# Kernel optimization log

Measured on AMD Instinct MI355X. Metric: run time of the kernel, lower is better.

Reference implementation:

```python
import jax, jax.numpy as jnp
import numpy as np

N_VERT = 1000          # num_of_vertices; x has 3*N_VERT rows
B = 32                 # batch
IN_DIM = 64
OUT_DIMS = [64, 64, 64]


def setup_inputs() -> dict:
    key = jax.random.key(0)
    ks = jax.random.split(key, 8)
    threeN = 3 * N_VERT
    x = jax.random.normal(ks[0], (threeN, B, IN_DIM), dtype=jnp.float32)
    # dense (normalized-ish) adjacency over the localized spatio-temporal graph
    adj = jax.random.uniform(ks[1], (threeN, threeN), dtype=jnp.float32) / threeN
    inp = {"x": x, "adj": adj}
    in_d = IN_DIM
    for i, out_d in enumerate(OUT_DIMS):
        # torch Linear(in_d, 2*out_d): store as [in_d, 2*out_d] for x @ W + b
        scale = 1.0 / np.sqrt(in_d)
        inp[f"W{i}"] = jax.random.uniform(ks[2 + 2 * i], (in_d, 2 * out_d),
                                          minval=-scale, maxval=scale, dtype=jnp.float32)
        inp[f"b{i}"] = jax.random.uniform(ks[3 + 2 * i], (2 * out_d,),
                                          minval=-scale, maxval=scale, dtype=jnp.float32)
        in_d = out_d
    return inp


def _gcn_glu(adj, x, W, b, out_dim):
    # aggregate: [3N,3N] x [3N,B,C] -> [3N,B,C]
    h = jnp.einsum('nm,mbc->nbc', adj, x)
    lr = h @ W + b                       # [3N,B,2*out]
    lhs, rhs = lr[..., :out_dim], lr[..., out_dim:]
    return lhs * jax.nn.sigmoid(rhs)     # GLU


def reference(x, adj, W0, b0, W1, b1, W2, b2):
    n = x.shape[0] // 3
    Ws = [(W0, b0), (W1, b1), (W2, b2)]
    mids = []
    h = x
    for (W, b), out_d in zip(Ws, OUT_DIMS):
        h = _gcn_glu(adj, h, W, b, out_d)
        mids.append(h[n:2 * n])          # middle time-step slice [N,B,out]
    return jnp.max(jnp.stack(mids, axis=0), axis=0)  # [N,B,out]
```

## Files before the change

kernel.cpp:

```cpp
#include <hip/hip_runtime.h>
#include <stdint.h>
#include <math.h>

#define NV   3000
#define MP   3072
#define NBC  2048
#define NMID 1000

typedef unsigned short u16;
typedef short  s8vec __attribute__((ext_vector_type(8)));
typedef float  f4vec __attribute__((ext_vector_type(4)));


__device__ __forceinline__ u16 f2b(float f) {
  union { float f; unsigned int u; } v; v.f = f;
  unsigned int r = v.u + 0x7FFFu + ((v.u >> 16) & 1u);
  return (u16)(r >> 16);
}
__device__ __forceinline__ float b2f(u16 u) {
  union { unsigned int u; float f; } v; v.u = ((unsigned int)u) << 16;
  return v.f;
}

__device__ __forceinline__ void gload16(const void* g, void* l) {
  __builtin_amdgcn_global_load_lds(
      (const __attribute__((address_space(1))) void*)g,
      (__attribute__((address_space(3))) void*)l, 16, 0, 0);
}

__global__ void k_conv_adj(const float* __restrict__ adj,
                           u16* __restrict__ adjt) {
  __shared__ __align__(16) u16 tb[64][80];
  const int bx = blockIdx.x;
  const int by = blockIdx.y;
  const int t  = threadIdx.x;

  {
    const int rl = t >> 2, quad = t & 3;
    const int r  = by * 64 + rl;
    const bool rok = (r < NV);
#pragma unroll
    for (int i = 0; i < 4; ++i) {
      int c = bx * 64 + quad * 16 + i * 4;
      float4 f = {0.f, 0.f, 0.f, 0.f};
      if (rok && c < NV) f = *(const float4*)(adj + (size_t)r * NV + c);
      ushort4 o;
      o.x = f2b(f.x); o.y = f2b(f.y); o.z = f2b(f.z); o.w = f2b(f.w);
      *(ushort4*)&tb[rl][quad * 16 + i * 4] = o;
    }
  }
  __syncthreads();

  {
#pragma unroll
    for (int h = 0; h < 2; ++h) {
      int chunk = t * 2 + h;
      int sel  = chunk >> 8;
      int g    = (chunk >> 6) & 3;
      int lane = chunk & 63;
      int row  = g * 16 + (lane & 15);
      int col  = sel * 32 + (lane >> 4) * 8;
      s8vec v = *(const s8vec*)&tb[row][col];
      size_t dst = ((size_t)(by * 96 + bx * 2 + sel) * 4 + g) * 512 + lane * 8;
      *(s8vec*)(adjt + dst) = v;
    }
  }
}

__global__ void k_conv_x(const float* __restrict__ x,
                         u16* __restrict__ xt) {
  __shared__ __align__(16) u16 tb[64][72];
  int t  = threadIdx.x;
  int k0 = blockIdx.x * 64;
  int n0 = blockIdx.y * 64;
  int kl = t >> 4, ch = t & 15;
#pragma unroll
  for (int r = 0; r < 4; ++r) {
    int k = k0 + kl + r * 16;
    float4 f = {0.f, 0.f, 0.f, 0.f};
    if (k < NV) f = *(const float4*)(x + (size_t)k * NBC + n0 + ch * 4);
    tb[ch * 4 + 0][kl + r * 16] = f2b(f.x);
    tb[ch * 4 + 1][kl + r * 16] = f2b(f.y);
    tb[ch * 4 + 2][kl + r * 16] = f2b(f.z);
    tb[ch * 4 + 3][kl + r * 16] = f2b(f.w);
  }
  __syncthreads();
  int nl = t >> 4, kc = t & 15;
#pragma unroll
  for (int r = 0; r < 4; ++r) {
    int n = n0 + nl + r * 16;
    int k = k0 + kc * 4;
    ushort4 o;
    o.x = tb[nl + r * 16][kc * 4 + 0];
    o.y = tb[nl + r * 16][kc * 4 + 1];
    o.z = tb[nl + r * 16][kc * 4 + 2];
    o.w = tb[nl + r * 16][kc * 4 + 3];
    int nt = n >> 7, g = (n >> 4) & 7, lr = n & 15;
    int kk = k >> 5, hi = (k >> 3) & 3, j = k & 7;
    size_t dst = ((size_t)(nt * 96 + kk) * 8 + g) * 512 +
                 (size_t)(hi * 16 + lr) * 8 + j;
    *(ushort4*)(xt + dst) = o;
  }
}

__global__ void k_conv_w(const float* __restrict__ W0,
                         const float* __restrict__ W1,
                         const float* __restrict__ W2,
                         u16* __restrict__ Wt) {
  int e = blockIdx.x * 256 + threadIdx.x;
  const float* W = (e < 8192) ? W0 : (e < 16384) ? W1 : W2;
  int r  = e & 8191;
  int kk = r >> 12, g = (r >> 9) & 7, ln = (r >> 3) & 63, jj = r & 7;
  int c = kk * 32 + (ln >> 4) * 8 + jj;
  int j = g * 16 + (ln & 15);
  Wt[e] = f2b(W[c * 128 + j]);
}

__global__ __launch_bounds__(256, 2) void k_gemm(
    const u16* __restrict__ At,
    const u16* __restrict__ Xt,
    u16* __restrict__ C0,
    u16* __restrict__ C1,
    int m64base,
    int nmt,
    int crow0,
    int chunk) {
  __shared__ __align__(16) u16 S[3 * 10240];

  const int bid = blockIdx.x;
  const int swz = (bid & 7) * chunk + (bid >> 3);
  const int nt  = swz & 15;
  const int mk  = swz >> 4;
  const int ks  = (mk >= nmt) ? 1 : 0;
  const int mt  = mk - ks * nmt;
  const int kt0 = ks * 48;

  const int tid  = threadIdx.x;
  const int w    = tid >> 6;
  const int lane = tid & 63;
  const int wr   = w >> 1;
  const int wc   = w & 1;

  const int c0 = w * 5;
  const u16* src[5];
  int stp[5];
#pragma unroll
  for (int i = 0; i < 5; ++i) {
    int c = c0 + i;
    if (c < 12) {
      int m64 = m64base + mt * 3 + (c >> 2);
      src[i] = At + ((size_t)(m64 * 96 + kt0) * 4 + (c & 3)) * 512 + lane * 8;
      stp[i] = 2048;
    } else {
      src[i] = Xt + ((size_t)(nt * 96 + kt0) * 8 + (c - 12)) * 512 + lane * 8;
      stp[i] = 4096;
    }
  }

  f4vec acc[6][4];
#pragma unroll
  for (int i = 0; i < 6; ++i)
#pragma unroll
    for (int j = 0; j < 4; ++j) acc[i][j] = (f4vec){0.f, 0.f, 0.f, 0.f};

  auto stage = [&](int buf, int t) {
    u16* d = S + buf * 10240 + c0 * 512;
#pragma unroll
    for (int i = 0; i < 5; ++i)
      gload16(src[i] + (size_t)t * stp[i], d + i * 512);
  };
  auto compute = [&](int buf) {
    const u16* Ab = S + buf * 10240 + (wr * 6) * 512 + lane * 8;
    const u16* Bb = S + buf * 10240 + 6144 + (wc * 4) * 512 + lane * 8;
    s8vec a[6], b[4];
#pragma unroll
    for (int mi = 0; mi < 6; ++mi)
      a[mi] = *(const s8vec*)(Ab + mi * 512);
#pragma unroll
    for (int ni = 0; ni < 4; ++ni)
      b[ni] = *(const s8vec*)(Bb + ni * 512);
#pragma unroll
    for (int mi = 0; mi < 6; ++mi)
#pragma unroll
      for (int ni = 0; ni < 4; ++ni)
        acc[mi][ni] = __builtin_amdgcn_mfma_f32_16x16x32_bf16(
            a[mi], b[ni], acc[mi][ni], 0, 0, 0);
  };

  stage(0, 0); stage(1, 1);

#pragma unroll 1
  for (int t = 0; t < 45; t += 3) {
#pragma unroll
    for (int u = 0; u < 3; ++u) {
      asm volatile("s_waitcnt vmcnt(5)" ::: "memory");
      asm volatile("s_barrier" ::: "memory");
      stage((u + 2) % 3, t + u + 2);
      compute(u);
    }
  }
  asm volatile("s_waitcnt vmcnt(5)" ::: "memory");
  asm volatile("s_barrier" ::: "memory");
  stage(2, 47);
  compute(0);
  asm volatile("s_waitcnt vmcnt(5)" ::: "memory");
  asm volatile("s_barrier" ::: "memory");
  compute(1);
  asm volatile("s_waitcnt vmcnt(0)" ::: "memory");
  asm volatile("s_barrier" ::: "memory");
  compute(2);

  u16* Cs = ks ? C1 : C0;
  const int rl = lane & 15;
  const int rh = lane >> 4;
  const int mrow0 = m64base * 64 + mt * 192 + wr * 96 - crow0;
#pragma unroll
  for (int mi = 0; mi < 6; ++mi)
#pragma unroll
    for (int ni = 0; ni < 4; ++ni) {
      int grow = mrow0 + mi * 16 + rh * 4;
      int gcol = nt * 128 + wc * 64 + ni * 16 + rl;
      u16* cp = Cs + (size_t)grow * NBC + gcol;
      cp[0 * NBC] = f2b(acc[mi][ni][0]);
      cp[1 * NBC] = f2b(acc[mi][ni][1]);
      cp[2 * NBC] = f2b(acc[mi][ni][2]);
      cp[3 * NBC] = f2b(acc[mi][ni][3]);
    }
}

template <int LAYER0, int WRITEX>
__global__ __launch_bounds__(256) void k_layerB(
    const u16* __restrict__ H0,
    const u16* __restrict__ H1,
    const u16* __restrict__ Wt,
    const float* __restrict__ bias,
    u16* __restrict__ xt,
    float* __restrict__ out,
    int vt0) {
  __shared__ __align__(16) u16 Hs[2][2][8][64][8];

  const int vt = vt0 + blockIdx.x;
  const int b  = blockIdx.y;
  const int v0 = vt * 128;
  const int t  = threadIdx.x;

#pragma unroll
  for (int h = 0; h < 2; ++h) {
    const u16* H = h ? H1 : H0;
#pragma unroll
    for (int q = 0; q < 4; ++q) {
      int id = q * 256 + t;
      int v  = id >> 3;
      int cc = (id & 7) * 8;
      s8vec hh = *(const s8vec*)(H + (size_t)(v0 + v) * NBC + b * 64 + cc);
      int kk = cc >> 5, g = v >> 4, ln = ((cc >> 3) & 3) * 16 + (v & 15);
      *(s8vec*)&Hs[h][kk][g][ln][0] = hh;
    }
  }
  __syncthreads();

  const int w    = t >> 6;
  const int lane = t & 63;
  const int wvh  = w >> 1;
  const int wc   = w & 1;

  s8vec bf[4][2];
#pragma unroll
  for (int ni = 0; ni < 4; ++ni) {
    int g = (ni < 2) ? (wc * 2 + ni) : (4 + wc * 2 + (ni - 2));
#pragma unroll
    for (int kk = 0; kk < 2; ++kk)
      bf[ni][kk] = *(const s8vec*)(Wt + ((size_t)(kk * 8 + g) * 64 + lane) * 8);
  }

  f4vec acc[4][4];
#pragma unroll
  for (int i = 0; i < 4; ++i)
#pragma unroll
    for (int j = 0; j < 4; ++j) acc[i][j] = (f4vec){0.f, 0.f, 0.f, 0.f};

#pragma unroll
  for (int h = 0; h < 2; ++h)
#pragma unroll
    for (int kk = 0; kk < 2; ++kk) {
      s8vec a[4];
#pragma unroll
      for (int mi = 0; mi < 4; ++mi)
        a[mi] = *(const s8vec*)&Hs[h][kk][wvh * 4 + mi][lane][0];
#pragma unroll
      for (int mi = 0; mi < 4; ++mi)
#pragma unroll
        for (int ni = 0; ni < 4; ++ni)
          acc[mi][ni] = __builtin_amdgcn_mfma_f32_16x16x32_bf16(
              a[mi], bf[ni][kk], acc[mi][ni], 0, 0, 0);
    }

  const int lr = lane & 15;
  const int rh = lane >> 4;
#pragma unroll
  for (int mi = 0; mi < 4; ++mi) {
    const int vbase = v0 + wvh * 64 + mi * 16 + rh * 4;
#pragma unroll
    for (int np = 0; np < 2; ++np) {
      const int j  = wc * 32 + np * 16 + lr;
      const float bl = bias[j];
      const float bh = bias[j + 64];
      float vals[4];
#pragma unroll
      for (int r = 0; r < 4; ++r) {
        float lo = acc[mi][np][r] + bl;
        float hi = acc[mi][np + 2][r] + bh;
        float gv = lo / (1.0f + __expf(-hi));
        vals[r] = ((vbase + r) < NV) ? gv : 0.0f;
      }
#pragma unroll
      for (int r = 0; r < 4; ++r) {
        int vg = vbase + r;
        if (vg >= NMID && vg < 2 * NMID) {
          size_t oi = (size_t)(vg - NMID) * NBC + b * 64 + j;
          if (LAYER0) out[oi] = vals[r];
          else        out[oi] = fmaxf(out[oi], vals[r]);
        }
      }
      if (WRITEX) {
        int n   = b * 64 + j;
        int nt  = n >> 7, g2 = (n >> 4) & 7, ln2 = n & 15;
        int kk2 = vbase >> 5, hi2 = (vbase >> 3) & 3, jj0 = vbase & 7;
        ushort4 o;
        o.x = f2b(vals[0]); o.y = f2b(vals[1]);
        o.z = f2b(vals[2]); o.w = f2b(vals[3]);
        size_t dst = ((size_t)(nt * 96 + kk2) * 8 + g2) * 512 +
                     (size_t)(hi2 * 16 + ln2) * 8 + jj0;
        *(ushort4*)(xt + dst) = o;
      }
    }
  }
}

extern "C" void kernel_launch(void* const* d_in, const int* in_sizes, int n_in,
                              void* d_out, int out_size, void* d_ws, size_t ws_size,
                              hipStream_t stream) {
  const float* x   = (const float*)d_in[0];
  const float* adj = (const float*)d_in[1];
  const float* W0  = (const float*)d_in[2];
  const float* b0  = (const float*)d_in[3];
  const float* W1  = (const float*)d_in[4];
  const float* b1  = (const float*)d_in[5];
  const float* W2  = (const float*)d_in[6];
  const float* b2  = (const float*)d_in[7];
  float* out = (float*)d_out;

  char* ws = (char*)d_ws;
  u16* adjt = (u16*)ws;
  u16* xa   = (u16*)(ws + 18874368);
  u16* xb   = (u16*)(ws + 18874368 + 12582912);
  u16* hb   = (u16*)(ws + 18874368 + 2 * 12582912);
  u16* Wt   = (u16*)(ws + 18874368 + 3 * 12582912);

  k_conv_adj<<<dim3(48, 48), 256, 0, stream>>>(adj, adjt);
  k_conv_x<<<dim3(48, 32), 256, 0, stream>>>(x, xa);
  k_conv_w<<<96, 256, 0, stream>>>(W0, W1, W2, Wt);

  k_gemm<<<512, 256, 0, stream>>>(adjt, xa, hb, xb, 0, 16, 0, 64);
  k_layerB<1, 1><<<dim3(24, 32), 256, 0, stream>>>(hb, xb, Wt, b0, xa, out, 0);
  k_gemm<<<512, 256, 0, stream>>>(adjt, xa, hb, xb, 0, 16, 0, 64);
  k_layerB<0, 1><<<dim3(24, 32), 256, 0, stream>>>(hb, xb, Wt + 8192, b1, xa, out, 0);
  k_gemm<<<192, 256, 0, stream>>>(adjt, xa, hb, xb, 14, 6, 896, 24);
  k_layerB<0, 0><<<dim3(9, 32), 256, 0, stream>>>(
      hb - (size_t)896 * NBC, xb - (size_t)896 * NBC, Wt + 16384, b2, xa, out, 7);
}
```

Baseline: 175.5 us.

## Load B operand directly into registers, stage only A through LDS

The GEMM kernel stops staging the X (B) tiles through shared memory. Each wave now loads its B fragments straight from global memory into a double-buffered register set one step ahead, while A tiles keep the triple-buffered LDS pipeline. This shrinks LDS use and LDS read traffic, which could allow more occupancy. The cost is more VGPRs and duplicated global B loads across the two wave rows, and the vmcnt accounting now has to cover both the direct loads and the async LDS loads.

```diff
diff --git a/kernel.cpp b/kernel.cpp
--- a/kernel.cpp
+++ b/kernel.cpp
@@ -125,7 +125,7 @@
     int nmt,
     int crow0,
     int chunk) {
-  __shared__ __align__(16) u16 S[3 * 10240];
+  __shared__ __align__(16) u16 S[3 * 6144];
 
   const int bid = blockIdx.x;
   const int swz = (bid & 7) * chunk + (bid >> 3);
@@ -141,21 +141,15 @@
   const int wr   = w >> 1;
   const int wc   = w & 1;
 
-  const int c0 = w * 5;
-  const u16* src[5];
-  int stp[5];
-#pragma unroll
-  for (int i = 0; i < 5; ++i) {
+  const int c0 = w * 3;
+  const u16* asrc[3];
+#pragma unroll
+  for (int i = 0; i < 3; ++i) {
     int c = c0 + i;
-    if (c < 12) {
-      int m64 = m64base + mt * 3 + (c >> 2);
-      src[i] = At + ((size_t)(m64 * 96 + kt0) * 4 + (c & 3)) * 512 + lane * 8;
-      stp[i] = 2048;
-    } else {
-      src[i] = Xt + ((size_t)(nt * 96 + kt0) * 8 + (c - 12)) * 512 + lane * 8;
-      stp[i] = 4096;
-    }
-  }
+    int m64 = m64base + mt * 3 + (c >> 2);
+    asrc[i] = At + ((size_t)(m64 * 96 + kt0) * 4 + (c & 3)) * 512 + lane * 8;
+  }
+  const u16* bsrc = Xt + ((size_t)(nt * 96 + kt0) * 8 + wc * 4) * 512 + lane * 8;
 
   f4vec acc[6][4];
 #pragma unroll
@@ -163,52 +157,75 @@
 #pragma unroll
     for (int j = 0; j < 4; ++j) acc[i][j] = (f4vec){0.f, 0.f, 0.f, 0.f};
 
-  auto stage = [&](int buf, int t) {
-    u16* d = S + buf * 10240 + c0 * 512;
-#pragma unroll
-    for (int i = 0; i < 5; ++i)
-      gload16(src[i] + (size_t)t * stp[i], d + i * 512);
+  s8vec breg[2][4];
+
+  auto stageA = [&](int buf, int t) {
+    u16* d = S + buf * 6144 + c0 * 512;
+#pragma unroll
+    for (int i = 0; i < 3; ++i)
+      gload16(asrc[i] + (size_t)t * 2048, d + i * 512);
   };
-  auto compute = [&](int buf) {
-    const u16* Ab = S + buf * 10240 + (wr * 6) * 512 + lane * 8;
-    const u16* Bb = S + buf * 10240 + 6144 + (wc * 4) * 512 + lane * 8;
-    s8vec a[6], b[4];
+  auto loadB = [&](int set, int t) {
+#pragma unroll
+    for (int ni = 0; ni < 4; ++ni)
+      breg[set][ni] = *(const s8vec*)(bsrc + (size_t)t * 4096 + ni * 512);
+  };
+  auto compute = [&](int buf, int set) {
+    const u16* Ab = S + buf * 6144 + (wr * 6) * 512 + lane * 8;
+    s8vec a[6];
 #pragma unroll
     for (int mi = 0; mi < 6; ++mi)
       a[mi] = *(const s8vec*)(Ab + mi * 512);
 #pragma unroll
-    for (int ni = 0; ni < 4; ++ni)
-      b[ni] = *(const s8vec*)(Bb + ni * 512);
-#pragma unroll
     for (int mi = 0; mi < 6; ++mi)
 #pragma unroll
       for (int ni = 0; ni < 4; ++ni)
         acc[mi][ni] = __builtin_amdgcn_mfma_f32_16x16x32_bf16(
-            a[mi], b[ni], acc[mi][ni], 0, 0, 0);
+            a[mi], breg[set][ni], acc[mi][ni], 0, 0, 0);
   };
 
-  stage(0, 0); stage(1, 1);
+  stageA(0, 0);
+  loadB(0, 0);
+  stageA(1, 1);
 
 #pragma unroll 1
-  for (int t = 0; t < 45; t += 3) {
-#pragma unroll
-    for (int u = 0; u < 3; ++u) {
-      asm volatile("s_waitcnt vmcnt(5)" ::: "memory");
+  for (int t = 0; t < 42; t += 6) {
+#pragma unroll
+    for (int u = 0; u < 6; ++u) {
+      asm volatile("s_waitcnt vmcnt(3)" ::: "memory");
+      loadB((u + 1) & 1, t + u + 1);
       asm volatile("s_barrier" ::: "memory");
-      stage((u + 2) % 3, t + u + 2);
-      compute(u);
-    }
-  }
-  asm volatile("s_waitcnt vmcnt(5)" ::: "memory");
-  asm volatile("s_barrier" ::: "memory");
-  stage(2, 47);
-  compute(0);
-  asm volatile("s_waitcnt vmcnt(5)" ::: "memory");
-  asm volatile("s_barrier" ::: "memory");
-  compute(1);
+      stageA((u + 2) % 3, t + u + 2);
+      compute(u % 3, u & 1);
+    }
+  }
+  asm volatile("s_waitcnt vmcnt(3)" ::: "memory");
+  loadB(1, 43);
+  asm volatile("s_barrier" ::: "memory");
+  stageA(2, 44);
+  compute(0, 0);
+  asm volatile("s_waitcnt vmcnt(3)" ::: "memory");
+  loadB(0, 44);
+  asm volatile("s_barrier" ::: "memory");
+  stageA(0, 45);
+  compute(1, 1);
+  asm volatile("s_waitcnt vmcnt(3)" ::: "memory");
+  loadB(1, 45);
+  asm volatile("s_barrier" ::: "memory");
+  stageA(1, 46);
+  compute(2, 0);
+  asm volatile("s_waitcnt vmcnt(3)" ::: "memory");
+  loadB(0, 46);
+  asm volatile("s_barrier" ::: "memory");
+  stageA(2, 47);
+  compute(0, 1);
+  asm volatile("s_waitcnt vmcnt(3)" ::: "memory");
+  loadB(1, 47);
+  asm volatile("s_barrier" ::: "memory");
+  compute(1, 0);
   asm volatile("s_waitcnt vmcnt(0)" ::: "memory");
   asm volatile("s_barrier" ::: "memory");
-  compute(2);
+  compute(2, 1);
 
   u16* Cs = ks ? C1 : C0;
   const int rl = lane & 15;
```

Result: slower. 182.6 us (+4.1%).

## Replace LDS-staged GEMM with direct register double-buffered loads and smaller tiles

Applied to the files above, without the earlier changes.

The adjacency GEMM no longer stages A/B tiles through shared memory with global_load_lds and barriers. Each wave now loads its own pre-swizzled fragments straight into registers with a two-set double buffer. The block tile shrinks from 192x128 to 128x128, raising grid size and occupancy (launch bounds 3), and MFMA sections get raised scheduling priority. This removes LDS traffic and barrier stalls, but operands are no longer shared across waves through LDS, so redundant global/L2 reads increase.

```diff
diff --git a/kernel.cpp b/kernel.cpp
--- a/kernel.cpp
+++ b/kernel.cpp
@@ -20,12 +20,6 @@
 __device__ __forceinline__ float b2f(u16 u) {
   union { unsigned int u; float f; } v; v.u = ((unsigned int)u) << 16;
   return v.f;
-}
-
-__device__ __forceinline__ void gload16(const void* g, void* l) {
-  __builtin_amdgcn_global_load_lds(
-      (const __attribute__((address_space(1))) void*)g,
-      (__attribute__((address_space(3))) void*)l, 16, 0, 0);
 }
 
 __global__ void k_conv_adj(const float* __restrict__ adj,
@@ -116,17 +110,16 @@
   Wt[e] = f2b(W[c * 128 + j]);
 }
 
-__global__ __launch_bounds__(256, 2) void k_gemm(
+template <int NKT>
+__global__ __launch_bounds__(256, 3) void k_gemm(
     const u16* __restrict__ At,
     const u16* __restrict__ Xt,
     u16* __restrict__ C0,
     u16* __restrict__ C1,
-    int m64base,
+    int mtbase,
     int nmt,
     int crow0,
     int chunk) {
-  __shared__ __align__(16) u16 S[3 * 10240];
-
   const int bid = blockIdx.x;
   const int swz = (bid & 7) * chunk + (bid >> 3);
   const int nt  = swz & 15;
@@ -141,81 +134,57 @@
   const int wr   = w >> 1;
   const int wc   = w & 1;
 
-  const int c0 = w * 5;
-  const u16* src[5];
-  int stp[5];
-#pragma unroll
-  for (int i = 0; i < 5; ++i) {
-    int c = c0 + i;
-    if (c < 12) {
-      int m64 = m64base + mt * 3 + (c >> 2);
-      src[i] = At + ((size_t)(m64 * 96 + kt0) * 4 + (c & 3)) * 512 + lane * 8;
-      stp[i] = 2048;
-    } else {
-      src[i] = Xt + ((size_t)(nt * 96 + kt0) * 8 + (c - 12)) * 512 + lane * 8;
-      stp[i] = 4096;
-    }
-  }
-
-  f4vec acc[6][4];
-#pragma unroll
-  for (int i = 0; i < 6; ++i)
+  const int m64 = (mtbase + mt) * 2 + wr;
+  const u16* abase = At + ((size_t)(m64 * 96 + kt0) * 4) * 512 + lane * 8;
+  const u16* bbase = Xt + ((size_t)(nt * 96 + kt0) * 8 + wc * 4) * 512 + lane * 8;
+
+  f4vec acc[4][4];
+#pragma unroll
+  for (int i = 0; i < 4; ++i)
 #pragma unroll
     for (int j = 0; j < 4; ++j) acc[i][j] = (f4vec){0.f, 0.f, 0.f, 0.f};
 
-  auto stage = [&](int buf, int t) {
-    u16* d = S + buf * 10240 + c0 * 512;
-#pragma unroll
-    for (int i = 0; i < 5; ++i)
-      gload16(src[i] + (size_t)t * stp[i], d + i * 512);
+  s8vec ar[2][4], br[2][4];
+
+  auto load = [&](int set, int s) {
+    const u16* ap = abase + (size_t)s * 2048;
+    const u16* bp = bbase + (size_t)s * 4096;
+#pragma unroll
+    for (int i = 0; i < 4; ++i)
+      ar[set][i] = *(const s8vec*)(ap + i * 512);
+#pragma unroll
+    for (int i = 0; i < 4; ++i)
+      br[set][i] = *(const s8vec*)(bp + i * 512);
   };
-  auto compute = [&](int buf) {
-    const u16* Ab = S + buf * 10240 + (wr * 6) * 512 + lane * 8;
-    const u16* Bb = S + buf * 10240 + 6144 + (wc * 4) * 512 + lane * 8;
-    s8vec a[6], b[4];
-#pragma unroll
-    for (int mi = 0; mi < 6; ++mi)
-      a[mi] = *(const s8vec*)(Ab + mi * 512);
-#pragma unroll
-    for (int ni = 0; ni < 4; ++ni)
-      b[ni] = *(const s8vec*)(Bb + ni * 512);
-#pragma unroll
-    for (int mi = 0; mi < 6; ++mi)
+  auto compute = [&](int set) {
+    __builtin_amdgcn_s_setprio(1);
+#pragma unroll
+    for (int mi = 0; mi < 4; ++mi)
 #pragma unroll
       for (int ni = 0; ni < 4; ++ni)
         acc[mi][ni] = __builtin_amdgcn_mfma_f32_16x16x32_bf16(
-            a[mi], b[ni], acc[mi][ni], 0, 0, 0);
+            ar[set][mi], br[set][ni], acc[mi][ni], 0, 0, 0);
+    __builtin_amdgcn_s_setprio(0);
   };
 
-  stage(0, 0); stage(1, 1);
-
+  load(0, 0);
 #pragma unroll 1
-  for (int t = 0; t < 45; t += 3) {
-#pragma unroll
-    for (int u = 0; u < 3; ++u) {
-      asm volatile("s_waitcnt vmcnt(5)" ::: "memory");
-      asm volatile("s_barrier" ::: "memory");
-      stage((u + 2) % 3, t + u + 2);
-      compute(u);
-    }
-  }
-  asm volatile("s_waitcnt vmcnt(5)" ::: "memory");
-  asm volatile("s_barrier" ::: "memory");
-  stage(2, 47);
+  for (int s = 0; s < NKT - 2; s += 2) {
+    load(1, s + 1);
+    compute(0);
+    load(0, s + 2);
+    compute(1);
+  }
+  load(1, NKT - 1);
   compute(0);
-  asm volatile("s_waitcnt vmcnt(5)" ::: "memory");
-  asm volatile("s_barrier" ::: "memory");
   compute(1);
-  asm volatile("s_waitcnt vmcnt(0)" ::: "memory");
-  asm volatile("s_barrier" ::: "memory");
-  compute(2);
 
   u16* Cs = ks ? C1 : C0;
   const int rl = lane & 15;
   const int rh = lane >> 4;
-  const int mrow0 = m64base * 64 + mt * 192 + wr * 96 - crow0;
-#pragma unroll
-  for (int mi = 0; mi < 6; ++mi)
+  const int mrow0 = (mtbase + mt) * 128 + wr * 64 - crow0;
+#pragma unroll
+  for (int mi = 0; mi < 4; ++mi)
 #pragma unroll
     for (int ni = 0; ni < 4; ++ni) {
       int grow = mrow0 + mi * 16 + rh * 4;
@@ -361,11 +330,11 @@
   k_conv_x<<<dim3(48, 32), 256, 0, stream>>>(x, xa);
   k_conv_w<<<96, 256, 0, stream>>>(W0, W1, W2, Wt);
 
-  k_gemm<<<512, 256, 0, stream>>>(adjt, xa, hb, xb, 0, 16, 0, 64);
+  k_gemm<48><<<768, 256, 0, stream>>>(adjt, xa, hb, xb, 0, 24, 0, 96);
   k_layerB<1, 1><<<dim3(24, 32), 256, 0, stream>>>(hb, xb, Wt, b0, xa, out, 0);
-  k_gemm<<<512, 256, 0, stream>>>(adjt, xa, hb, xb, 0, 16, 0, 64);
+  k_gemm<48><<<768, 256, 0, stream>>>(adjt, xa, hb, xb, 0, 24, 0, 96);
   k_layerB<0, 1><<<dim3(24, 32), 256, 0, stream>>>(hb, xb, Wt + 8192, b1, xa, out, 0);
-  k_gemm<<<192, 256, 0, stream>>>(adjt, xa, hb, xb, 14, 6, 896, 24);
+  k_gemm<48><<<288, 256, 0, stream>>>(adjt, xa, hb, xb, 7, 9, 896, 36);
   k_layerB<0, 0><<<dim3(9, 32), 256, 0, stream>>>(
       hb - (size_t)896 * NBC, xb - (size_t)896 * NBC, Wt + 16384, b2, xa, out, 7);
 }
```

Result: slower. 197.5 us (+12.5%).
